# Kernel optimization log

Measured on AMD Instinct MI355X. Metric: run time of the kernel, lower is better.

The kernel has to match this reference:

```python
import jax, jax.numpy as jnp
import numpy as np

IN_CH = 1024
INTER_CH = 512
NUM_EXPERTS = 128
B, S = 16, 4096  # T = B*S = 65536 tokens, 512 tokens/expert


def setup_inputs() -> dict:
    key = jax.random.key(0)
    kx, kp, k1w, k1b, k2w, k2b, k3w, k3b = jax.random.split(key, 8)
    T = B * S
    x = jax.random.normal(kx, (B, S, IN_CH), dtype=jnp.float32)
    # Mirror torch: indices = randperm(T) % E; idxs = indices.argsort() (stable)
    perm = jax.random.permutation(kp, T)
    expert_assign = perm % NUM_EXPERTS
    idxs = jnp.argsort(expert_assign, stable=True).astype(jnp.int64)
    # BatchLinear params initialized with randn, matching the torch module
    w1_w = jax.random.normal(k1w, (NUM_EXPERTS, INTER_CH, IN_CH), dtype=jnp.float32)
    w1_b = jax.random.normal(k1b, (NUM_EXPERTS, INTER_CH), dtype=jnp.float32)
    w2_w = jax.random.normal(k2w, (NUM_EXPERTS, IN_CH, INTER_CH), dtype=jnp.float32)
    w2_b = jax.random.normal(k2b, (NUM_EXPERTS, IN_CH), dtype=jnp.float32)
    w3_w = jax.random.normal(k3w, (NUM_EXPERTS, INTER_CH, IN_CH), dtype=jnp.float32)
    w3_b = jax.random.normal(k3b, (NUM_EXPERTS, INTER_CH), dtype=jnp.float32)
    return {"x": x, "idxs": idxs, "w1_w": w1_w, "w1_b": w1_b,
            "w2_w": w2_w, "w2_b": w2_b, "w3_w": w3_w, "w3_b": w3_b}


def reference(x, idxs, w1_w, w1_b, w2_w, w2_b, w3_w, w3_b):
    Bx, Sx, C = x.shape
    E = w1_w.shape[0]
    xf = x.reshape(Bx * Sx, C)            # [T, C]
    # dispatch: gather tokens grouped by expert -> [E, T/E, C]
    xs = xf[idxs].reshape(E, -1, C)
    # SwiGLU FFN, batched over experts
    h1 = jnp.einsum('etc,efc->etf', xs, w1_w) + w1_b[:, None, :]  # [E, T/E, F]
    h3 = jnp.einsum('etc,efc->etf', xs, w3_w) + w3_b[:, None, :]
    h = jax.nn.silu(h1) * h3
    out = jnp.einsum('etf,ecf->etc', h, w2_w) + w2_b[:, None, :]  # [E, T/E, C]
    # combine: scatter tokens back to original order
    out = out.reshape(Bx * Sx, C)
    inv = jnp.argsort(idxs)
    return out[inv].reshape(Bx, Sx, C)
```

## Files before the change

### kernel.cpp

```cpp
#include <hip/hip_runtime.h>

#define IN_CH 1024
#define INTER 512
#define NEXP  128
#define TPE   512

typedef __bf16 bf16x8  __attribute__((ext_vector_type(8)));
typedef __bf16 bf16x4v __attribute__((ext_vector_type(4)));
typedef float  f32x4   __attribute__((ext_vector_type(4)));

__global__ __launch_bounds__(512) void moe_h_kernel(
    const float* __restrict__ x, const int* __restrict__ idxs,
    const float* __restrict__ w1w, const float* __restrict__ w1b,
    const float* __restrict__ w3w, const float* __restrict__ w3b,
    __bf16* __restrict__ hbuf)
{
  __shared__ __align__(16) ushort sA [2][128*64];
  __shared__ __align__(16) ushort sB1[2][128*64];
  __shared__ __align__(16) ushort sB3[2][128*64];

  const int blk = (blockIdx.x & 7) * (NEXP*16/8) + (blockIdx.x >> 3);
  const int e   = blk >> 4;
  const int tl  = blk & 15;
  const int tm  = tl >> 2, tn = tl & 3;

  const int tid  = threadIdx.x;
  const int lane = tid & 63;
  const int wid  = tid >> 6;
  const int wm   = wid >> 1;
  const int wn   = wid & 1;

  const int r0 = tid >> 4;
  const int c4 = tid & 15;

  const float* aptr[4];
#pragma unroll
  for (int i = 0; i < 4; ++i) {
    const int tok = idxs[e*TPE + tm*128 + r0 + 32*i];
    aptr[i] = x + (size_t)tok*IN_CH + (c4<<2);
  }
  const float* b1p = w1w + ((size_t)e*INTER + tn*128 + r0)*IN_CH + (c4<<2);
  const float* b3p = w3w + ((size_t)e*INTER + tn*128 + r0)*IN_CH + (c4<<2);

  const int swz = ((((c4>>1) ^ (r0&7))<<3) | ((c4&1)<<2));

  f32x4 acc1[2][4], acc3[2][4];
#pragma unroll
  for (int a = 0; a < 2; ++a)
#pragma unroll
    for (int b = 0; b < 4; ++b) {
      acc1[a][b] = (f32x4){0.f,0.f,0.f,0.f};
      acc3[a][b] = (f32x4){0.f,0.f,0.f,0.f};
    }

  float4 xv[4], v1[4], v3[4];

  auto loads = [&](int kof) {
#pragma unroll
    for (int i = 0; i < 4; ++i) {
      xv[i] = *(const float4*)(aptr[i] + kof);
      v1[i] = *(const float4*)(b1p + (size_t)(32*i)*IN_CH + kof);
      v3[i] = *(const float4*)(b3p + (size_t)(32*i)*IN_CH + kof);
    }
  };
  auto stores = [&](int buf) {
#pragma unroll
    for (int i = 0; i < 4; ++i) {
      const int ro = (r0 + 32*i)*64 + swz;
      bf16x4v a, b, c;
      a[0]=(__bf16)xv[i].x; a[1]=(__bf16)xv[i].y; a[2]=(__bf16)xv[i].z; a[3]=(__bf16)xv[i].w;
      b[0]=(__bf16)v1[i].x; b[1]=(__bf16)v1[i].y; b[2]=(__bf16)v1[i].z; b[3]=(__bf16)v1[i].w;
      c[0]=(__bf16)v3[i].x; c[1]=(__bf16)v3[i].y; c[2]=(__bf16)v3[i].z; c[3]=(__bf16)v3[i].w;
      *(bf16x4v*)&sA [buf][ro] = a;
      *(bf16x4v*)&sB1[buf][ro] = b;
      *(bf16x4v*)&sB3[buf][ro] = c;
    }
  };
  auto mfma_tile = [&](int buf) {
#pragma unroll
    for (int ks = 0; ks < 2; ++ks) {
      bf16x8 af[2], bq[4], bt[4];
      const int k8 = (ks<<2) + (lane>>4);
#pragma unroll
      for (int mi = 0; mi < 2; ++mi) {
        const int r = wm*32 + mi*16 + (lane&15);
        af[mi] = *(const bf16x8*)&sA[buf][r*64 + ((k8 ^ (r&7))<<3)];
      }
#pragma unroll
      for (int ni = 0; ni < 4; ++ni) {
        const int r   = wn*64 + ni*16 + (lane&15);
        const int off = r*64 + ((k8 ^ (r&7))<<3);
        bq[ni] = *(const bf16x8*)&sB1[buf][off];
        bt[ni] = *(const bf16x8*)&sB3[buf][off];
      }
#pragma unroll
      for (int mi = 0; mi < 2; ++mi)
#pragma unroll
        for (int ni = 0; ni < 4; ++ni) {
          acc1[mi][ni] = __builtin_amdgcn_mfma_f32_16x16x32_bf16(af[mi], bq[ni], acc1[mi][ni], 0, 0, 0);
          acc3[mi][ni] = __builtin_amdgcn_mfma_f32_16x16x32_bf16(af[mi], bt[ni], acc3[mi][ni], 0, 0, 0);
        }
    }
  };

  loads(0);
  stores(0);
  loads(64);
  asm volatile("s_waitcnt lgkmcnt(0)" ::: "memory");
  __builtin_amdgcn_s_barrier();

  int cur = 0;
  for (int kt = 0; kt < IN_CH/64; ++kt) {
    if (kt < IN_CH/64 - 1) {
      stores(cur ^ 1);
      if (kt < IN_CH/64 - 2) loads((kt+2)*64);
    }
    __builtin_amdgcn_s_setprio(1);
    mfma_tile(cur);
    __builtin_amdgcn_s_setprio(0);
    asm volatile("s_waitcnt lgkmcnt(0)" ::: "memory");
    __builtin_amdgcn_s_barrier();
    cur ^= 1;
  }

  const int rowbase = tm*128 + wm*32;
  const int colbase = tn*128 + wn*64;
#pragma unroll
  for (int ni = 0; ni < 4; ++ni) {
    const int fc = colbase + ni*16 + (lane&15);
    const float b1v = w1b[e*INTER + fc];
    const float b3v = w3b[e*INTER + fc];
#pragma unroll
    for (int mi = 0; mi < 2; ++mi) {
#pragma unroll
      for (int j = 0; j < 4; ++j) {
        const int rl = rowbase + mi*16 + ((lane>>4)<<2) + j;
        const float h1 = acc1[mi][ni][j] + b1v;
        const float h3 = acc3[mi][ni][j] + b3v;
        const float s  = h1 / (1.0f + __expf(-h1));
        hbuf[((size_t)e*TPE + rl)*INTER + fc] = (__bf16)(s * h3);
      }
    }
  }
}

__global__ __launch_bounds__(512) void moe_out_kernel(
    const __bf16* __restrict__ hbuf, const float* __restrict__ w2w,
    const float* __restrict__ w2b, const int* __restrict__ idxs,
    float* __restrict__ out)
{
  __shared__ __align__(16) ushort sA[2][128*64];
  __shared__ __align__(16) ushort sB[2][128*64];

  const int blk = (blockIdx.x & 7) * (NEXP*32/8) + (blockIdx.x >> 3);
  const int e   = blk >> 5;
  const int tl  = blk & 31;
  const int tm  = tl >> 3, tn = tl & 7;

  const int tid  = threadIdx.x;
  const int lane = tid & 63;
  const int wid  = tid >> 6;
  const int wm   = wid >> 1;
  const int wn   = wid & 1;

  const int rA   = tid >> 3;
  const int c8   = tid & 7;
  const int swzA = ((c8 ^ (rA&7))<<3);
  const __bf16* ap = hbuf + ((size_t)e*TPE + tm*128 + rA)*INTER + (c8<<3);

  const int r0   = tid >> 4;
  const int c4   = tid & 15;
  const int swzB = ((((c4>>1) ^ (r0&7))<<3) | ((c4&1)<<2));
  const float* bp = w2w + ((size_t)e*IN_CH + tn*128 + r0)*INTER + (c4<<2);

  f32x4 acc[2][4];
#pragma unroll
  for (int a = 0; a < 2; ++a)
#pragma unroll
    for (int b = 0; b < 4; ++b) acc[a][b] = (f32x4){0.f,0.f,0.f,0.f};

  uint4  hv[2];
  float4 wv[4];

  auto loads = [&](int kof) {
#pragma unroll
    for (int i = 0; i < 2; ++i)
      hv[i] = *(const uint4*)(ap + (size_t)(64*i)*INTER + kof);
#pragma unroll
    for (int i = 0; i < 4; ++i)
      wv[i] = *(const float4*)(bp + (size_t)(32*i)*INTER + kof);
  };
  auto stores = [&](int buf) {
#pragma unroll
    for (int i = 0; i < 2; ++i)
      *(uint4*)&sA[buf][(rA + 64*i)*64 + swzA] = hv[i];
#pragma unroll
    for (int i = 0; i < 4; ++i) {
      bf16x4v b;
      b[0]=(__bf16)wv[i].x; b[1]=(__bf16)wv[i].y; b[2]=(__bf16)wv[i].z; b[3]=(__bf16)wv[i].w;
      *(bf16x4v*)&sB[buf][(r0 + 32*i)*64 + swzB] = b;
    }
  };
  auto mfma_tile = [&](int buf) {
#pragma unroll
    for (int ks = 0; ks < 2; ++ks) {
      bf16x8 af[2], bf[4];
      const int k8 = (ks<<2) + (lane>>4);
#pragma unroll
      for (int mi = 0; mi < 2; ++mi) {
        const int r = wm*32 + mi*16 + (lane&15);
        af[mi] = *(const bf16x8*)&sA[buf][r*64 + ((k8 ^ (r&7))<<3)];
      }
#pragma unroll
      for (int ni = 0; ni < 4; ++ni) {
        const int r = wn*64 + ni*16 + (lane&15);
        bf[ni] = *(const bf16x8*)&sB[buf][r*64 + ((k8 ^ (r&7))<<3)];
      }
#pragma unroll
      for (int mi = 0; mi < 2; ++mi)
#pragma unroll
        for (int ni = 0; ni < 4; ++ni)
          acc[mi][ni] = __builtin_amdgcn_mfma_f32_16x16x32_bf16(af[mi], bf[ni], acc[mi][ni], 0, 0, 0);
    }
  };

  loads(0);
  stores(0);
  loads(64);
  asm volatile("s_waitcnt lgkmcnt(0)" ::: "memory");
  __builtin_amdgcn_s_barrier();

  int cur = 0;
  for (int kt = 0; kt < INTER/64; ++kt) {
    if (kt < INTER/64 - 1) {
      stores(cur ^ 1);
      if (kt < INTER/64 - 2) loads((kt+2)*64);
    }
    __builtin_amdgcn_s_setprio(1);
    mfma_tile(cur);
    __builtin_amdgcn_s_setprio(0);
    asm volatile("s_waitcnt lgkmcnt(0)" ::: "memory");
    __builtin_amdgcn_s_barrier();
    cur ^= 1;
  }

  const int rowbase = tm*128 + wm*32;
  const int colbase = tn*128 + wn*64;
  float b2v[4];
#pragma unroll
  for (int ni = 0; ni < 4; ++ni)
    b2v[ni] = w2b[e*IN_CH + colbase + ni*16 + (lane&15)];
#pragma unroll
  for (int mi = 0; mi < 2; ++mi) {
#pragma unroll
    for (int j = 0; j < 4; ++j) {
      const int rl  = rowbase + mi*16 + ((lane>>4)<<2) + j;
      const int tok = idxs[e*TPE + rl];
      float* orow = out + (size_t)tok*IN_CH;
#pragma unroll
      for (int ni = 0; ni < 4; ++ni)
        orow[colbase + ni*16 + (lane&15)] = acc[mi][ni][j] + b2v[ni];
    }
  }
}

extern "C" void kernel_launch(void* const* d_in, const int* in_sizes, int n_in,
                              void* d_out, int out_size, void* d_ws, size_t ws_size,
                              hipStream_t stream) {
  const float* x    = (const float*)d_in[0];
  const int*   idxs = (const int*)d_in[1];
  const float* w1w  = (const float*)d_in[2];
  const float* w1b  = (const float*)d_in[3];
  const float* w2w  = (const float*)d_in[4];
  const float* w2b  = (const float*)d_in[5];
  const float* w3w  = (const float*)d_in[6];
  const float* w3b  = (const float*)d_in[7];
  float*  out  = (float*)d_out;
  __bf16* hbuf = (__bf16*)d_ws;

  moe_h_kernel<<<dim3(NEXP*16), dim3(512), 0, stream>>>(x, idxs, w1w, w1b, w3w, w3b, hbuf);
  moe_out_kernel<<<dim3(NEXP*32), dim3(512), 0, stream>>>(hbuf, w2w, w2b, idxs, out);
}
```

Measured before the change: 490.5 us.

## Halve K-tile to 32 and request higher occupancy in both MoE GEMM kernels

Both GEMM kernels shrink the shared-memory K tile from 64 to 32 bf16 columns, which halves LDS use and the per-thread staging registers. The global-to-LDS load mapping is reworked so each thread loads one row's 8 contiguous elements and stores them as a single 16-byte write with a 4-way XOR swizzle. Launch bounds now request 4 blocks per CU to raise occupancy. In exchange there are twice as many K iterations and barriers, and each iteration does half as much MFMA work to hide load latency behind.

```diff
diff --git a/kernel.cpp b/kernel.cpp
--- a/kernel.cpp
+++ b/kernel.cpp
@@ -6,18 +6,17 @@
 #define TPE   512
 
 typedef __bf16 bf16x8  __attribute__((ext_vector_type(8)));
-typedef __bf16 bf16x4v __attribute__((ext_vector_type(4)));
 typedef float  f32x4   __attribute__((ext_vector_type(4)));
 
-__global__ __launch_bounds__(512) void moe_h_kernel(
+__global__ __launch_bounds__(512, 4) void moe_h_kernel(
     const float* __restrict__ x, const int* __restrict__ idxs,
     const float* __restrict__ w1w, const float* __restrict__ w1b,
     const float* __restrict__ w3w, const float* __restrict__ w3b,
     __bf16* __restrict__ hbuf)
 {
-  __shared__ __align__(16) ushort sA [2][128*64];
-  __shared__ __align__(16) ushort sB1[2][128*64];
-  __shared__ __align__(16) ushort sB3[2][128*64];
+  __shared__ __align__(16) ushort sA [2][128*32];
+  __shared__ __align__(16) ushort sB1[2][128*32];
+  __shared__ __align__(16) ushort sB3[2][128*32];
 
   const int blk = (blockIdx.x & 7) * (NEXP*16/8) + (blockIdx.x >> 3);
   const int e   = blk >> 4;
@@ -30,19 +29,14 @@
   const int wm   = wid >> 1;
   const int wn   = wid & 1;
 
-  const int r0 = tid >> 4;
-  const int c4 = tid & 15;
-
-  const float* aptr[4];
-#pragma unroll
-  for (int i = 0; i < 4; ++i) {
-    const int tok = idxs[e*TPE + tm*128 + r0 + 32*i];
-    aptr[i] = x + (size_t)tok*IN_CH + (c4<<2);
-  }
-  const float* b1p = w1w + ((size_t)e*INTER + tn*128 + r0)*IN_CH + (c4<<2);
-  const float* b3p = w3w + ((size_t)e*INTER + tn*128 + r0)*IN_CH + (c4<<2);
-
-  const int swz = ((((c4>>1) ^ (r0&7))<<3) | ((c4&1)<<2));
+  const int row = tid >> 2;
+  const int c   = tid & 3;
+  const int sro = row*32 + ((c ^ (row&3))<<3);
+
+  const int tok = idxs[e*TPE + tm*128 + row];
+  const float* ap  = x   + (size_t)tok*IN_CH + (c<<3);
+  const float* b1p = w1w + ((size_t)e*INTER + tn*128 + row)*IN_CH + (c<<3);
+  const float* b3p = w3w + ((size_t)e*INTER + tn*128 + row)*IN_CH + (c<<3);
 
   f32x4 acc1[2][4], acc3[2][4];
 #pragma unroll
@@ -53,67 +47,63 @@
       acc3[a][b] = (f32x4){0.f,0.f,0.f,0.f};
     }
 
-  float4 xv[4], v1[4], v3[4];
+  float4 xa, xb, w1a, w1b_, w3a, w3b_;
 
   auto loads = [&](int kof) {
-#pragma unroll
-    for (int i = 0; i < 4; ++i) {
-      xv[i] = *(const float4*)(aptr[i] + kof);
-      v1[i] = *(const float4*)(b1p + (size_t)(32*i)*IN_CH + kof);
-      v3[i] = *(const float4*)(b3p + (size_t)(32*i)*IN_CH + kof);
-    }
+    xa   = *(const float4*)(ap  + kof);
+    xb   = *(const float4*)(ap  + kof + 4);
+    w1a  = *(const float4*)(b1p + kof);
+    w1b_ = *(const float4*)(b1p + kof + 4);
+    w3a  = *(const float4*)(b3p + kof);
+    w3b_ = *(const float4*)(b3p + kof + 4);
+  };
+  auto cvt8 = [](const float4& lo, const float4& hi) {
+    bf16x8 r;
+    r[0]=(__bf16)lo.x; r[1]=(__bf16)lo.y; r[2]=(__bf16)lo.z; r[3]=(__bf16)lo.w;
+    r[4]=(__bf16)hi.x; r[5]=(__bf16)hi.y; r[6]=(__bf16)hi.z; r[7]=(__bf16)hi.w;
+    return r;
   };
   auto stores = [&](int buf) {
-#pragma unroll
-    for (int i = 0; i < 4; ++i) {
-      const int ro = (r0 + 32*i)*64 + swz;
-      bf16x4v a, b, c;
-      a[0]=(__bf16)xv[i].x; a[1]=(__bf16)xv[i].y; a[2]=(__bf16)xv[i].z; a[3]=(__bf16)xv[i].w;
-      b[0]=(__bf16)v1[i].x; b[1]=(__bf16)v1[i].y; b[2]=(__bf16)v1[i].z; b[3]=(__bf16)v1[i].w;
-      c[0]=(__bf16)v3[i].x; c[1]=(__bf16)v3[i].y; c[2]=(__bf16)v3[i].z; c[3]=(__bf16)v3[i].w;
-      *(bf16x4v*)&sA [buf][ro] = a;
-      *(bf16x4v*)&sB1[buf][ro] = b;
-      *(bf16x4v*)&sB3[buf][ro] = c;
-    }
+    *(bf16x8*)&sA [buf][sro] = cvt8(xa,  xb);
+    *(bf16x8*)&sB1[buf][sro] = cvt8(w1a, w1b_);
+    *(bf16x8*)&sB3[buf][sro] = cvt8(w3a, w3b_);
   };
   auto mfma_tile = [&](int buf) {
-#pragma unroll
-    for (int ks = 0; ks < 2; ++ks) {
-      bf16x8 af[2], bq[4], bt[4];
-      const int k8 = (ks<<2) + (lane>>4);
-#pragma unroll
-      for (int mi = 0; mi < 2; ++mi) {
-        const int r = wm*32 + mi*16 + (lane&15);
-        af[mi] = *(const bf16x8*)&sA[buf][r*64 + ((k8 ^ (r&7))<<3)];
+    bf16x8 af[2], bq[4], bt[4];
+    const int k8 = lane>>4;
+#pragma unroll
+    for (int mi = 0; mi < 2; ++mi) {
+      const int r = wm*32 + mi*16 + (lane&15);
+      af[mi] = *(const bf16x8*)&sA[buf][r*32 + ((k8 ^ (r&3))<<3)];
+    }
+#pragma unroll
+    for (int ni = 0; ni < 4; ++ni) {
+      const int r   = wn*64 + ni*16 + (lane&15);
+      const int off = r*32 + ((k8 ^ (r&3))<<3);
+      bq[ni] = *(const bf16x8*)&sB1[buf][off];
+      bt[ni] = *(const bf16x8*)&sB3[buf][off];
+    }
+#pragma unroll
+    for (int mi = 0; mi < 2; ++mi)
+#pragma unroll
+      for (int ni = 0; ni < 4; ++ni) {
+        acc1[mi][ni] = __builtin_amdgcn_mfma_f32_16x16x32_bf16(af[mi], bq[ni], acc1[mi][ni], 0, 0, 0);
+        acc3[mi][ni] = __builtin_amdgcn_mfma_f32_16x16x32_bf16(af[mi], bt[ni], acc3[mi][ni], 0, 0, 0);
       }
-#pragma unroll
-      for (int ni = 0; ni < 4; ++ni) {
-        const int r   = wn*64 + ni*16 + (lane&15);
-        const int off = r*64 + ((k8 ^ (r&7))<<3);
-        bq[ni] = *(const bf16x8*)&sB1[buf][off];
-        bt[ni] = *(const bf16x8*)&sB3[buf][off];
-      }
-#pragma unroll
-      for (int mi = 0; mi < 2; ++mi)
-#pragma unroll
-        for (int ni = 0; ni < 4; ++ni) {
-          acc1[mi][ni] = __builtin_amdgcn_mfma_f32_16x16x32_bf16(af[mi], bq[ni], acc1[mi][ni], 0, 0, 0);
-          acc3[mi][ni] = __builtin_amdgcn_mfma_f32_16x16x32_bf16(af[mi], bt[ni], acc3[mi][ni], 0, 0, 0);
-        }
-    }
   };
 
   loads(0);
   stores(0);
-  loads(64);
+  loads(32);
   asm volatile("s_waitcnt lgkmcnt(0)" ::: "memory");
   __builtin_amdgcn_s_barrier();
 
   int cur = 0;
-  for (int kt = 0; kt < IN_CH/64; ++kt) {
-    if (kt < IN_CH/64 - 1) {
+  const int NT = IN_CH/32;
+  for (int kt = 0; kt < NT; ++kt) {
+    if (kt < NT - 1) {
       stores(cur ^ 1);
-      if (kt < IN_CH/64 - 2) loads((kt+2)*64);
+      if (kt < NT - 2) loads((kt+2)*32);
     }
     __builtin_amdgcn_s_setprio(1);
     mfma_tile(cur);
@@ -144,13 +134,13 @@
   }
 }
 
-__global__ __launch_bounds__(512) void moe_out_kernel(
+__global__ __launch_bounds__(512, 4) void moe_out_kernel(
     const __bf16* __restrict__ hbuf, const float* __restrict__ w2w,
     const float* __restrict__ w2b, const int* __restrict__ idxs,
     float* __restrict__ out)
 {
-  __shared__ __align__(16) ushort sA[2][128*64];
-  __shared__ __align__(16) ushort sB[2][128*64];
+  __shared__ __align__(16) ushort sA[2][128*32];
+  __shared__ __align__(16) ushort sB[2][128*32];
 
   const int blk = (blockIdx.x & 7) * (NEXP*32/8) + (blockIdx.x >> 3);
   const int e   = blk >> 5;
@@ -163,15 +153,12 @@
   const int wm   = wid >> 1;
   const int wn   = wid & 1;
 
-  const int rA   = tid >> 3;
-  const int c8   = tid & 7;
-  const int swzA = ((c8 ^ (rA&7))<<3);
-  const __bf16* ap = hbuf + ((size_t)e*TPE + tm*128 + rA)*INTER + (c8<<3);
-
-  const int r0   = tid >> 4;
-  const int c4   = tid & 15;
-  const int swzB = ((((c4>>1) ^ (r0&7))<<3) | ((c4&1)<<2));
-  const float* bp = w2w + ((size_t)e*IN_CH + tn*128 + r0)*INTER + (c4<<2);
+  const int row = tid >> 2;
+  const int c   = tid & 3;
+  const int sro = row*32 + ((c ^ (row&3))<<3);
+
+  const __bf16* ap = hbuf + ((size_t)e*TPE + tm*128 + row)*INTER + (c<<3);
+  const float*  bp = w2w + ((size_t)e*IN_CH + tn*128 + row)*INTER + (c<<3);
 
   f32x4 acc[2][4];
 #pragma unroll
@@ -179,62 +166,53 @@
 #pragma unroll
     for (int b = 0; b < 4; ++b) acc[a][b] = (f32x4){0.f,0.f,0.f,0.f};
 
-  uint4  hv[2];
-  float4 wv[4];
+  uint4  hv;
+  float4 wa, wb;
 
   auto loads = [&](int kof) {
-#pragma unroll
-    for (int i = 0; i < 2; ++i)
-      hv[i] = *(const uint4*)(ap + (size_t)(64*i)*INTER + kof);
-#pragma unroll
-    for (int i = 0; i < 4; ++i)
-      wv[i] = *(const float4*)(bp + (size_t)(32*i)*INTER + kof);
+    hv = *(const uint4*)(ap + kof);
+    wa = *(const float4*)(bp + kof);
+    wb = *(const float4*)(bp + kof + 4);
   };
   auto stores = [&](int buf) {
-#pragma unroll
-    for (int i = 0; i < 2; ++i)
-      *(uint4*)&sA[buf][(rA + 64*i)*64 + swzA] = hv[i];
-#pragma unroll
-    for (int i = 0; i < 4; ++i) {
-      bf16x4v b;
-      b[0]=(__bf16)wv[i].x; b[1]=(__bf16)wv[i].y; b[2]=(__bf16)wv[i].z; b[3]=(__bf16)wv[i].w;
-      *(bf16x4v*)&sB[buf][(r0 + 32*i)*64 + swzB] = b;
-    }
+    *(uint4*)&sA[buf][sro] = hv;
+    bf16x8 r;
+    r[0]=(__bf16)wa.x; r[1]=(__bf16)wa.y; r[2]=(__bf16)wa.z; r[3]=(__bf16)wa.w;
+    r[4]=(__bf16)wb.x; r[5]=(__bf16)wb.y; r[6]=(__bf16)wb.z; r[7]=(__bf16)wb.w;
+    *(bf16x8*)&sB[buf][sro] = r;
   };
   auto mfma_tile = [&](int buf) {
-#pragma unroll
-    for (int ks = 0; ks < 2; ++ks) {
-      bf16x8 af[2], bf[4];
-      const int k8 = (ks<<2) + (lane>>4);
-#pragma unroll
-      for (int mi = 0; mi < 2; ++mi) {
-        const int r = wm*32 + mi*16 + (lane&15);
-        af[mi] = *(const bf16x8*)&sA[buf][r*64 + ((k8 ^ (r&7))<<3)];
-      }
-#pragma unroll
-      for (int ni = 0; ni < 4; ++ni) {
-        const int r = wn*64 + ni*16 + (lane&15);
-        bf[ni] = *(const bf16x8*)&sB[buf][r*64 + ((k8 ^ (r&7))<<3)];
-      }
-#pragma unroll
-      for (int mi = 0; mi < 2; ++mi)
-#pragma unroll
-        for (int ni = 0; ni < 4; ++ni)
-          acc[mi][ni] = __builtin_amdgcn_mfma_f32_16x16x32_bf16(af[mi], bf[ni], acc[mi][ni], 0, 0, 0);
-    }
+    bf16x8 af[2], bf[4];
+    const int k8 = lane>>4;
+#pragma unroll
+    for (int mi = 0; mi < 2; ++mi) {
+      const int r = wm*32 + mi*16 + (lane&15);
+      af[mi] = *(const bf16x8*)&sA[buf][r*32 + ((k8 ^ (r&3))<<3)];
+    }
+#pragma unroll
+    for (int ni = 0; ni < 4; ++ni) {
+      const int r = wn*64 + ni*16 + (lane&15);
+      bf[ni] = *(const bf16x8*)&sB[buf][r*32 + ((k8 ^ (r&3))<<3)];
+    }
+#pragma unroll
+    for (int mi = 0; mi < 2; ++mi)
+#pragma unroll
+      for (int ni = 0; ni < 4; ++ni)
+        acc[mi][ni] = __builtin_amdgcn_mfma_f32_16x16x32_bf16(af[mi], bf[ni], acc[mi][ni], 0, 0, 0);
   };
 
   loads(0);
   stores(0);
-  loads(64);
+  loads(32);
   asm volatile("s_waitcnt lgkmcnt(0)" ::: "memory");
   __builtin_amdgcn_s_barrier();
 
   int cur = 0;
-  for (int kt = 0; kt < INTER/64; ++kt) {
-    if (kt < INTER/64 - 1) {
+  const int NT = INTER/32;
+  for (int kt = 0; kt < NT; ++kt) {
+    if (kt < NT - 1) {
       stores(cur ^ 1);
-      if (kt < INTER/64 - 2) loads((kt+2)*64);
+      if (kt < NT - 2) loads((kt+2)*32);
     }
     __builtin_amdgcn_s_setprio(1);
     mfma_tile(cur);
```

Measured after the change: 859.8 us. 1.75x slower.

## Split GEMM main loops into barrier-separated phases interleaving LDS reads with MFMA

Applied to the files above, without the earlier changes.

Both expert GEMM kernels now split each K-tile into several phases (4 in the gate/up kernel, 2 in the down kernel). Each phase issues its LDS fragment reads plus a slice of the global loads or LDS stores, then runs a barrier, lgkmcnt wait, sched_barrier and raised priority before its block of MFMAs. This is a ping-pong style schedule meant to stagger waves so that memory and MFMA work from different waves overlap better. The cost is many more workgroup barriers per tile, which can add stall time if the waves do not stay evenly staggered.

```diff
diff --git a/kernel.cpp b/kernel.cpp
--- a/kernel.cpp
+++ b/kernel.cpp
@@ -6,8 +6,16 @@
 #define TPE   512
 
 typedef __bf16 bf16x8  __attribute__((ext_vector_type(8)));
-typedef __bf16 bf16x4v __attribute__((ext_vector_type(4)));
 typedef float  f32x4   __attribute__((ext_vector_type(4)));
+
+#define PHASE_SYNC() do { \
+  __builtin_amdgcn_s_barrier(); \
+  asm volatile("s_waitcnt lgkmcnt(0)" ::: "memory"); \
+  __builtin_amdgcn_sched_barrier(0); \
+  __builtin_amdgcn_s_setprio(1); } while (0)
+#define PHASE_END() do { \
+  __builtin_amdgcn_s_setprio(0); \
+  __builtin_amdgcn_s_barrier(); } while (0)
 
 __global__ __launch_bounds__(512) void moe_h_kernel(
     const float* __restrict__ x, const int* __restrict__ idxs,
@@ -67,6 +75,7 @@
 #pragma unroll
     for (int i = 0; i < 4; ++i) {
       const int ro = (r0 + 32*i)*64 + swz;
+      typedef __bf16 bf16x4v __attribute__((ext_vector_type(4)));
       bf16x4v a, b, c;
       a[0]=(__bf16)xv[i].x; a[1]=(__bf16)xv[i].y; a[2]=(__bf16)xv[i].z; a[3]=(__bf16)xv[i].w;
       b[0]=(__bf16)v1[i].x; b[1]=(__bf16)v1[i].y; b[2]=(__bf16)v1[i].z; b[3]=(__bf16)v1[i].w;
@@ -76,30 +85,22 @@
       *(bf16x4v*)&sB3[buf][ro] = c;
     }
   };
-  auto mfma_tile = [&](int buf) {
-#pragma unroll
-    for (int ks = 0; ks < 2; ++ks) {
-      bf16x8 af[2], bq[4], bt[4];
-      const int k8 = (ks<<2) + (lane>>4);
-#pragma unroll
-      for (int mi = 0; mi < 2; ++mi) {
-        const int r = wm*32 + mi*16 + (lane&15);
-        af[mi] = *(const bf16x8*)&sA[buf][r*64 + ((k8 ^ (r&7))<<3)];
-      }
-#pragma unroll
-      for (int ni = 0; ni < 4; ++ni) {
-        const int r   = wn*64 + ni*16 + (lane&15);
-        const int off = r*64 + ((k8 ^ (r&7))<<3);
-        bq[ni] = *(const bf16x8*)&sB1[buf][off];
-        bt[ni] = *(const bf16x8*)&sB3[buf][off];
-      }
-#pragma unroll
-      for (int mi = 0; mi < 2; ++mi)
-#pragma unroll
-        for (int ni = 0; ni < 4; ++ni) {
-          acc1[mi][ni] = __builtin_amdgcn_mfma_f32_16x16x32_bf16(af[mi], bq[ni], acc1[mi][ni], 0, 0, 0);
-          acc3[mi][ni] = __builtin_amdgcn_mfma_f32_16x16x32_bf16(af[mi], bt[ni], acc3[mi][ni], 0, 0, 0);
-        }
+  auto rdA = [&](int buf, int ks, bf16x8 af[2]) {
+    const int k8 = (ks<<2) + (lane>>4);
+#pragma unroll
+    for (int mi = 0; mi < 2; ++mi) {
+      const int r = wm*32 + mi*16 + (lane&15);
+      af[mi] = *(const bf16x8*)&sA[buf][r*64 + ((k8 ^ (r&7))<<3)];
+    }
+  };
+  auto rdB = [&](int buf, int ks, int nh, bf16x8 bq[2], bf16x8 bt[2]) {
+    const int k8 = (ks<<2) + (lane>>4);
+#pragma unroll
+    for (int nl = 0; nl < 2; ++nl) {
+      const int r   = wn*64 + (nh*2 + nl)*16 + (lane&15);
+      const int off = r*64 + ((k8 ^ (r&7))<<3);
+      bq[nl] = *(const bf16x8*)&sB1[buf][off];
+      bt[nl] = *(const bf16x8*)&sB3[buf][off];
     }
   };
 
@@ -110,16 +111,58 @@
   __builtin_amdgcn_s_barrier();
 
   int cur = 0;
-  for (int kt = 0; kt < IN_CH/64; ++kt) {
-    if (kt < IN_CH/64 - 1) {
-      stores(cur ^ 1);
-      if (kt < IN_CH/64 - 2) loads((kt+2)*64);
-    }
-    __builtin_amdgcn_s_setprio(1);
-    mfma_tile(cur);
-    __builtin_amdgcn_s_setprio(0);
-    asm volatile("s_waitcnt lgkmcnt(0)" ::: "memory");
-    __builtin_amdgcn_s_barrier();
+  const int NT = IN_CH/64;
+  for (int kt = 0; kt < NT; ++kt) {
+    bf16x8 af[2], bq[2], bt[2];
+
+    rdA(cur, 0, af);
+    rdB(cur, 0, 0, bq, bt);
+    PHASE_SYNC();
+#pragma unroll
+    for (int mi = 0; mi < 2; ++mi)
+#pragma unroll
+      for (int nl = 0; nl < 2; ++nl) {
+        acc1[mi][nl] = __builtin_amdgcn_mfma_f32_16x16x32_bf16(af[mi], bq[nl], acc1[mi][nl], 0, 0, 0);
+        acc3[mi][nl] = __builtin_amdgcn_mfma_f32_16x16x32_bf16(af[mi], bt[nl], acc3[mi][nl], 0, 0, 0);
+      }
+    PHASE_END();
+
+    rdB(cur, 0, 1, bq, bt);
+    PHASE_SYNC();
+#pragma unroll
+    for (int mi = 0; mi < 2; ++mi)
+#pragma unroll
+      for (int nl = 0; nl < 2; ++nl) {
+        acc1[mi][2+nl] = __builtin_amdgcn_mfma_f32_16x16x32_bf16(af[mi], bq[nl], acc1[mi][2+nl], 0, 0, 0);
+        acc3[mi][2+nl] = __builtin_amdgcn_mfma_f32_16x16x32_bf16(af[mi], bt[nl], acc3[mi][2+nl], 0, 0, 0);
+      }
+    PHASE_END();
+
+    rdA(cur, 1, af);
+    rdB(cur, 1, 0, bq, bt);
+    if (kt < NT - 1) stores(cur ^ 1);
+    PHASE_SYNC();
+#pragma unroll
+    for (int mi = 0; mi < 2; ++mi)
+#pragma unroll
+      for (int nl = 0; nl < 2; ++nl) {
+        acc1[mi][nl] = __builtin_amdgcn_mfma_f32_16x16x32_bf16(af[mi], bq[nl], acc1[mi][nl], 0, 0, 0);
+        acc3[mi][nl] = __builtin_amdgcn_mfma_f32_16x16x32_bf16(af[mi], bt[nl], acc3[mi][nl], 0, 0, 0);
+      }
+    PHASE_END();
+
+    rdB(cur, 1, 1, bq, bt);
+    if (kt < NT - 2) loads((kt+2)*64);
+    PHASE_SYNC();
+#pragma unroll
+    for (int mi = 0; mi < 2; ++mi)
+#pragma unroll
+      for (int nl = 0; nl < 2; ++nl) {
+        acc1[mi][2+nl] = __builtin_amdgcn_mfma_f32_16x16x32_bf16(af[mi], bq[nl], acc1[mi][2+nl], 0, 0, 0);
+        acc3[mi][2+nl] = __builtin_amdgcn_mfma_f32_16x16x32_bf16(af[mi], bt[nl], acc3[mi][2+nl], 0, 0, 0);
+      }
+    PHASE_END();
+
     cur ^= 1;
   }
 
@@ -196,31 +239,26 @@
       *(uint4*)&sA[buf][(rA + 64*i)*64 + swzA] = hv[i];
 #pragma unroll
     for (int i = 0; i < 4; ++i) {
+      typedef __bf16 bf16x4v __attribute__((ext_vector_type(4)));
       bf16x4v b;
       b[0]=(__bf16)wv[i].x; b[1]=(__bf16)wv[i].y; b[2]=(__bf16)wv[i].z; b[3]=(__bf16)wv[i].w;
       *(bf16x4v*)&sB[buf][(r0 + 32*i)*64 + swzB] = b;
     }
   };
-  auto mfma_tile = [&](int buf) {
-#pragma unroll
-    for (int ks = 0; ks < 2; ++ks) {
-      bf16x8 af[2], bf[4];
-      const int k8 = (ks<<2) + (lane>>4);
-#pragma unroll
-      for (int mi = 0; mi < 2; ++mi) {
-        const int r = wm*32 + mi*16 + (lane&15);
-        af[mi] = *(const bf16x8*)&sA[buf][r*64 + ((k8 ^ (r&7))<<3)];
-      }
-#pragma unroll
-      for (int ni = 0; ni < 4; ++ni) {
-        const int r = wn*64 + ni*16 + (lane&15);
-        bf[ni] = *(const bf16x8*)&sB[buf][r*64 + ((k8 ^ (r&7))<<3)];
-      }
-#pragma unroll
-      for (int mi = 0; mi < 2; ++mi)
-#pragma unroll
-        for (int ni = 0; ni < 4; ++ni)
-          acc[mi][ni] = __builtin_amdgcn_mfma_f32_16x16x32_bf16(af[mi], bf[ni], acc[mi][ni], 0, 0, 0);
+  auto rdA = [&](int buf, int ks, bf16x8 af[2]) {
+    const int k8 = (ks<<2) + (lane>>4);
+#pragma unroll
+    for (int mi = 0; mi < 2; ++mi) {
+      const int r = wm*32 + mi*16 + (lane&15);
+      af[mi] = *(const bf16x8*)&sA[buf][r*64 + ((k8 ^ (r&7))<<3)];
+    }
+  };
+  auto rdB = [&](int buf, int ks, bf16x8 bfr[4]) {
+    const int k8 = (ks<<2) + (lane>>4);
+#pragma unroll
+    for (int ni = 0; ni < 4; ++ni) {
+      const int r = wn*64 + ni*16 + (lane&15);
+      bfr[ni] = *(const bf16x8*)&sB[buf][r*64 + ((k8 ^ (r&7))<<3)];
     }
   };
 
@@ -231,16 +269,32 @@
   __builtin_amdgcn_s_barrier();
 
   int cur = 0;
-  for (int kt = 0; kt < INTER/64; ++kt) {
-    if (kt < INTER/64 - 1) {
-      stores(cur ^ 1);
-      if (kt < INTER/64 - 2) loads((kt+2)*64);
-    }
-    __builtin_amdgcn_s_setprio(1);
-    mfma_tile(cur);
-    __builtin_amdgcn_s_setprio(0);
-    asm volatile("s_waitcnt lgkmcnt(0)" ::: "memory");
-    __builtin_amdgcn_s_barrier();
+  const int NT = INTER/64;
+  for (int kt = 0; kt < NT; ++kt) {
+    bf16x8 af[2], bfr[4];
+
+    rdA(cur, 0, af);
+    rdB(cur, 0, bfr);
+    if (kt < NT - 1) stores(cur ^ 1);
+    PHASE_SYNC();
+#pragma unroll
+    for (int mi = 0; mi < 2; ++mi)
+#pragma unroll
+      for (int ni = 0; ni < 4; ++ni)
+        acc[mi][ni] = __builtin_amdgcn_mfma_f32_16x16x32_bf16(af[mi], bfr[ni], acc[mi][ni], 0, 0, 0);
+    PHASE_END();
+
+    rdA(cur, 1, af);
+    rdB(cur, 1, bfr);
+    if (kt < NT - 2) loads((kt+2)*64);
+    PHASE_SYNC();
+#pragma unroll
+    for (int mi = 0; mi < 2; ++mi)
+#pragma unroll
+      for (int ni = 0; ni < 4; ++ni)
+        acc[mi][ni] = __builtin_amdgcn_mfma_f32_16x16x32_bf16(af[mi], bfr[ni], acc[mi][ni], 0, 0, 0);
+    PHASE_END();
+
     cur ^= 1;
   }
 
```

Result: slower. 527.6 us (+7.6%).

## Use inline-asm global loads and split down-proj K loop into synchronized phases

Applied to the files above, without the earlier changes.

The gate/up kernel now issues its global loads as inline-asm dwordx4 loads, with an explicit vmcnt wait before converting and storing to LDS. This keeps the compiler from reordering or merging those loads. The down-projection loop is split into two half-K phases. Each phase interleaves LDS fragment reads with either the LDS stores or the next global loads, and is bracketed by barriers and priority changes. The aim is to overlap memory traffic with MFMA work more deterministically, at the cost of extra barriers per K step and a full vmcnt(0) stall before each LDS store.

```diff
diff --git a/kernel.cpp b/kernel.cpp
--- a/kernel.cpp
+++ b/kernel.cpp
@@ -8,6 +8,22 @@
 typedef __bf16 bf16x8  __attribute__((ext_vector_type(8)));
 typedef __bf16 bf16x4v __attribute__((ext_vector_type(4)));
 typedef float  f32x4   __attribute__((ext_vector_type(4)));
+
+#define GLOAD(dst, p) \
+  asm volatile("global_load_dwordx4 %0, %1, off" : "=&v"(dst) : "v"(p))
+
+#define VM_WAIT() do { \
+  asm volatile("s_waitcnt vmcnt(0)" ::: "memory"); \
+  __builtin_amdgcn_sched_barrier(0); } while (0)
+
+#define PHASE_SYNC() do { \
+  __builtin_amdgcn_s_barrier(); \
+  asm volatile("s_waitcnt lgkmcnt(0)" ::: "memory"); \
+  __builtin_amdgcn_sched_barrier(0); \
+  __builtin_amdgcn_s_setprio(1); } while (0)
+#define PHASE_END() do { \
+  __builtin_amdgcn_s_setprio(0); \
+  __builtin_amdgcn_s_barrier(); } while (0)
 
 __global__ __launch_bounds__(512) void moe_h_kernel(
     const float* __restrict__ x, const int* __restrict__ idxs,
@@ -53,27 +69,29 @@
       acc3[a][b] = (f32x4){0.f,0.f,0.f,0.f};
     }
 
-  float4 xv[4], v1[4], v3[4];
+  f32x4 xv[4], v1[4], v3[4];
 
   auto loads = [&](int kof) {
 #pragma unroll
     for (int i = 0; i < 4; ++i) {
-      xv[i] = *(const float4*)(aptr[i] + kof);
-      v1[i] = *(const float4*)(b1p + (size_t)(32*i)*IN_CH + kof);
-      v3[i] = *(const float4*)(b3p + (size_t)(32*i)*IN_CH + kof);
-    }
+      GLOAD(xv[i], aptr[i] + kof);
+      GLOAD(v1[i], b1p + (size_t)(32*i)*IN_CH + kof);
+      GLOAD(v3[i], b3p + (size_t)(32*i)*IN_CH + kof);
+    }
+  };
+  auto cvt4 = [](const f32x4& v) {
+    bf16x4v b;
+    b[0]=(__bf16)v[0]; b[1]=(__bf16)v[1]; b[2]=(__bf16)v[2]; b[3]=(__bf16)v[3];
+    return b;
   };
   auto stores = [&](int buf) {
+    VM_WAIT();
 #pragma unroll
     for (int i = 0; i < 4; ++i) {
       const int ro = (r0 + 32*i)*64 + swz;
-      bf16x4v a, b, c;
-      a[0]=(__bf16)xv[i].x; a[1]=(__bf16)xv[i].y; a[2]=(__bf16)xv[i].z; a[3]=(__bf16)xv[i].w;
-      b[0]=(__bf16)v1[i].x; b[1]=(__bf16)v1[i].y; b[2]=(__bf16)v1[i].z; b[3]=(__bf16)v1[i].w;
-      c[0]=(__bf16)v3[i].x; c[1]=(__bf16)v3[i].y; c[2]=(__bf16)v3[i].z; c[3]=(__bf16)v3[i].w;
-      *(bf16x4v*)&sA [buf][ro] = a;
-      *(bf16x4v*)&sB1[buf][ro] = b;
-      *(bf16x4v*)&sB3[buf][ro] = c;
+      *(bf16x4v*)&sA [buf][ro] = cvt4(xv[i]);
+      *(bf16x4v*)&sB1[buf][ro] = cvt4(v1[i]);
+      *(bf16x4v*)&sB3[buf][ro] = cvt4(v3[i]);
     }
   };
   auto mfma_tile = [&](int buf) {
@@ -110,11 +128,10 @@
   __builtin_amdgcn_s_barrier();
 
   int cur = 0;
-  for (int kt = 0; kt < IN_CH/64; ++kt) {
-    if (kt < IN_CH/64 - 1) {
-      stores(cur ^ 1);
-      if (kt < IN_CH/64 - 2) loads((kt+2)*64);
-    }
+  const int NT = IN_CH/64;
+  for (int kt = 0; kt < NT; ++kt) {
+    if (kt < NT - 1) stores(cur ^ 1);
+    if (kt < NT - 2) loads((kt+2)*64);
     __builtin_amdgcn_s_setprio(1);
     mfma_tile(cur);
     __builtin_amdgcn_s_setprio(0);
@@ -201,26 +218,20 @@
       *(bf16x4v*)&sB[buf][(r0 + 32*i)*64 + swzB] = b;
     }
   };
-  auto mfma_tile = [&](int buf) {
-#pragma unroll
-    for (int ks = 0; ks < 2; ++ks) {
-      bf16x8 af[2], bf[4];
-      const int k8 = (ks<<2) + (lane>>4);
-#pragma unroll
-      for (int mi = 0; mi < 2; ++mi) {
-        const int r = wm*32 + mi*16 + (lane&15);
-        af[mi] = *(const bf16x8*)&sA[buf][r*64 + ((k8 ^ (r&7))<<3)];
-      }
-#pragma unroll
-      for (int ni = 0; ni < 4; ++ni) {
-        const int r = wn*64 + ni*16 + (lane&15);
-        bf[ni] = *(const bf16x8*)&sB[buf][r*64 + ((k8 ^ (r&7))<<3)];
-      }
-#pragma unroll
-      for (int mi = 0; mi < 2; ++mi)
-#pragma unroll
-        for (int ni = 0; ni < 4; ++ni)
-          acc[mi][ni] = __builtin_amdgcn_mfma_f32_16x16x32_bf16(af[mi], bf[ni], acc[mi][ni], 0, 0, 0);
+  auto rdA = [&](int buf, int ks, bf16x8 af[2]) {
+    const int k8 = (ks<<2) + (lane>>4);
+#pragma unroll
+    for (int mi = 0; mi < 2; ++mi) {
+      const int r = wm*32 + mi*16 + (lane&15);
+      af[mi] = *(const bf16x8*)&sA[buf][r*64 + ((k8 ^ (r&7))<<3)];
+    }
+  };
+  auto rdB = [&](int buf, int ks, bf16x8 bfr[4]) {
+    const int k8 = (ks<<2) + (lane>>4);
+#pragma unroll
+    for (int ni = 0; ni < 4; ++ni) {
+      const int r = wn*64 + ni*16 + (lane&15);
+      bfr[ni] = *(const bf16x8*)&sB[buf][r*64 + ((k8 ^ (r&7))<<3)];
     }
   };
 
@@ -231,16 +242,32 @@
   __builtin_amdgcn_s_barrier();
 
   int cur = 0;
-  for (int kt = 0; kt < INTER/64; ++kt) {
-    if (kt < INTER/64 - 1) {
-      stores(cur ^ 1);
-      if (kt < INTER/64 - 2) loads((kt+2)*64);
-    }
-    __builtin_amdgcn_s_setprio(1);
-    mfma_tile(cur);
-    __builtin_amdgcn_s_setprio(0);
-    asm volatile("s_waitcnt lgkmcnt(0)" ::: "memory");
-    __builtin_amdgcn_s_barrier();
+  const int NT = INTER/64;
+  for (int kt = 0; kt < NT; ++kt) {
+    bf16x8 af[2], bfr[4];
+
+    rdA(cur, 0, af);
+    rdB(cur, 0, bfr);
+    if (kt < NT - 1) stores(cur ^ 1);
+    PHASE_SYNC();
+#pragma unroll
+    for (int mi = 0; mi < 2; ++mi)
+#pragma unroll
+      for (int ni = 0; ni < 4; ++ni)
+        acc[mi][ni] = __builtin_amdgcn_mfma_f32_16x16x32_bf16(af[mi], bfr[ni], acc[mi][ni], 0, 0, 0);
+    PHASE_END();
+
+    rdA(cur, 1, af);
+    rdB(cur, 1, bfr);
+    if (kt < NT - 2) loads((kt+2)*64);
+    PHASE_SYNC();
+#pragma unroll
+    for (int mi = 0; mi < 2; ++mi)
+#pragma unroll
+      for (int ni = 0; ni < 4; ++ni)
+        acc[mi][ni] = __builtin_amdgcn_mfma_f32_16x16x32_bf16(af[mi], bfr[ni], acc[mi][ni], 0, 0, 0);
+    PHASE_END();
+
     cur ^= 1;
   }
 
```

New measurement: 490.2 us. About the same (-0.1%).
